# Kernel optimization log

Measured on AMD Instinct MI355X. Metric: run time of the kernel, lower is better.

The kernel has to match this reference:

```python
import jax, jax.numpy as jnp
import numpy as np

N_NODES = 100000
N_EDGES = 1600000
IN_DIM, HID_DIM, OUT_DIM = 64, 128, 1


def gcn_conv(x, W, b, src, dst, n_nodes):
    """PyG-style GCNConv: h = x @ W; out = D^-1/2 (A+I) D^-1/2 h + b.
    Self-loops handled analytically (message h_i * dinv_i^2) to avoid
    concatenating them onto the edge list."""
    h = x @ W  # [N, F_out]
    ones = jnp.ones((src.shape[0],), dtype=x.dtype)
    deg = jax.ops.segment_sum(ones, dst, num_segments=n_nodes) + 1.0  # +1 self-loop
    dinv = jax.lax.rsqrt(deg)  # deg >= 1 so always finite
    norm = dinv[src] * dinv[dst]  # [E]
    msgs = h[src] * norm[:, None]  # [E, F_out] gather + scale
    agg = jax.ops.segment_sum(msgs, dst, num_segments=n_nodes)  # scatter-add
    agg = agg + h * (dinv * dinv)[:, None]  # self-loop contribution
    return agg + b


def setup_inputs() -> dict:
    key = jax.random.key(0)
    k1, k2, k3, k4 = jax.random.split(key, 4)
    x = jax.random.normal(k1, (N_NODES, IN_DIM), dtype=jnp.float32)
    edge_index = jax.random.randint(k2, (2, N_EDGES), 0, N_NODES, dtype=jnp.int64)
    # Glorot-ish init for weights
    W1 = jax.random.normal(k3, (IN_DIM, HID_DIM), dtype=jnp.float32) / np.sqrt(IN_DIM)
    b1 = jnp.zeros((HID_DIM,), dtype=jnp.float32)
    W2 = jax.random.normal(k4, (HID_DIM, OUT_DIM), dtype=jnp.float32) / np.sqrt(HID_DIM)
    b2 = jnp.zeros((OUT_DIM,), dtype=jnp.float32)
    return {"x": x, "edge_index": edge_index, "W1": W1, "b1": b1, "W2": W2, "b2": b2}


def reference(x, edge_index, W1, b1, W2, b2):
    src, dst = edge_index[0], edge_index[1]
    h = gcn_conv(x, W1, b1, src, dst, N_NODES)
    h = jax.nn.relu(h)
    # dropout(0.3) in eval mode == identity
    out = gcn_conv(h, W2, b2, src, dst, N_NODES)
    return out.reshape(-1)  # [N]
```

## Files before the change

kernel.cpp:

```cpp
#include <hip/hip_runtime.h>
#include <hip/hip_bf16.h>

#define NNODES 100000
#define NEDGES 1600000
#define IN_DIM 64
#define HID_DIM 128

#define BUKSHIFT 7
#define BUKNODES 128
#define NBUK ((NNODES + 127) >> 7)
#define BUKCAP 2432
#define CHUNK 4096
#define TILE_N 128
#define W1TS 72
#define ACCS 66
#define QS 4096.0f

#define EPACK(s, d)  ((s) | (((d) & 127) << 24))
#define ESRC(p)      ((p) & 0x00FFFFFF)
#define EDL(p)       ((int)(((unsigned)(p)) >> 24))

typedef __attribute__((ext_vector_type(8))) short short8;
typedef __attribute__((ext_vector_type(4))) float f32x4;

__device__ inline unsigned short f2bf(float f) {
    unsigned u = __float_as_uint(f);
    u += 0x7fff + ((u >> 16) & 1);
    return (unsigned short)(u >> 16);
}
__device__ inline unsigned bfpack2(float a, float b) {
    return (unsigned)f2bf(a) | ((unsigned)f2bf(b) << 16);
}
__device__ inline int f2i12(float v) {
    float c = fminf(fmaxf(v * QS, -32767.f), 32767.f);
    return __float2int_rn(c);
}

__global__ __launch_bounds__(1024, 8) void k_part(const int* __restrict__ src,
                                                  const int* __restrict__ dst,
                                                  int* __restrict__ gbcur,
                                                  int* __restrict__ ebuf, int E) {
    __shared__ int stage[CHUNK];
    __shared__ unsigned short bukof[CHUNK];
    __shared__ int hist[NBUK];
    __shared__ int scanb[NBUK];
    __shared__ int basep[NBUK];
    __shared__ int sb[2][1024];
    int t = threadIdx.x;
    int start = blockIdx.x * CHUNK;
    int n = E - start; if (n > CHUNK) n = CHUNK;

    if (t < NBUK) hist[t] = 0;
    __syncthreads();

    int myb[4], myr[4], mp[4];
    #pragma unroll
    for (int i = 0; i < 4; i++) {
        int c = t + i * 1024;
        if (c < n) {
            int s = src[start + c];
            int d = dst[start + c];
            int b = d >> BUKSHIFT;
            myb[i] = b;
            mp[i]  = EPACK(s, d);
            myr[i] = atomicAdd(&hist[b], 1);
        } else myb[i] = -1;
    }
    __syncthreads();

    {
        int v = (t < NBUK) ? hist[t] : 0;
        sb[0][t] = v;
        __syncthreads();
        int pin = 0;
        for (int ofs = 1; ofs < 1024; ofs <<= 1) {
            sb[pin ^ 1][t] = (t >= ofs) ? sb[pin][t] + sb[pin][t - ofs] : sb[pin][t];
            __syncthreads();
            pin ^= 1;
        }
        if (t < NBUK) scanb[t] = sb[pin][t] - v;
    }

    if (t < NBUK) {
        int h = hist[t];
        basep[t] = h ? (t * BUKCAP + atomicAdd(&gbcur[t], h)) : 0;
    }
    __syncthreads();

    #pragma unroll
    for (int i = 0; i < 4; i++) {
        if (myb[i] >= 0) {
            int p = scanb[myb[i]] + myr[i];
            stage[p] = mp[i];
            bukof[p] = (unsigned short)myb[i];
        }
    }
    __syncthreads();

    for (int c = t; c < n; c += 1024) {
        int b = bukof[c];
        ebuf[basep[b] + (c - scanb[b])] = stage[c];
    }
}

__global__ __launch_bounds__(1024, 8) void k_bfill(const int* __restrict__ gbcur,
                                                   const int* __restrict__ ebuf,
                                                   const float* __restrict__ x,
                                                   int* __restrict__ off,
                                                   int* __restrict__ nend,
                                                   float* __restrict__ dinv,
                                                   int* __restrict__ csr,
                                                   short* __restrict__ xsq, int N) {
    __shared__ int sEdge[BUKCAP];
    __shared__ int lcnt[BUKNODES];
    __shared__ int sbuf[2][BUKNODES];
    __shared__ int cur[BUKNODES];
    __shared__ float sdinv[BUKNODES];
    int b = blockIdx.x, t = threadIdx.x;
    int nbase = b << BUKSHIFT;
    int rbase = b * BUKCAP;
    int cntb = gbcur[b];
    if (t < BUKNODES) lcnt[t] = 0;
    __syncthreads();
    for (int i = t; i < cntb; i += 1024) {
        int p = ebuf[rbase + i];
        sEdge[i] = p;
        atomicAdd(&lcnt[EDL(p)], 1);
    }
    __syncthreads();
    int v = (t < BUKNODES) ? lcnt[t] : 0;
    if (t < BUKNODES) sbuf[0][t] = v;
    __syncthreads();
    int pin = 0;
    for (int ofs = 1; ofs < BUKNODES; ofs <<= 1) {
        if (t < BUKNODES) sbuf[pin ^ 1][t] = (t >= ofs) ? sbuf[pin][t] + sbuf[pin][t - ofs]
                                                        : sbuf[pin][t];
        __syncthreads();
        pin ^= 1;
    }
    if (t < BUKNODES) {
        int o = rbase + sbuf[pin][t] - v;
        int nid = nbase + t;
        float dv = rsqrtf((float)v + 1.0f);
        sdinv[t] = dv;
        if (nid < N) {
            off[nid]  = o;
            nend[nid] = o + v;
            dinv[nid] = dv;
        }
        cur[t] = o;
    }
    __syncthreads();
    for (int i = t; i < cntb; i += 1024) {
        int p = sEdge[i];
        int pos = atomicAdd(&cur[EDL(p)], 1);
        csr[pos] = ESRC(p);
    }
    for (int i = t; i < BUKNODES * 16; i += 1024) {
        int nl = i >> 4;
        int nid = nbase + nl;
        if (nid < N) {
            float dv = sdinv[nl];
            float4 vx = ((const float4*)x)[(size_t)nid * 16 + (i & 15)];
            int q0 = f2i12(vx.x * dv), q1 = f2i12(vx.y * dv);
            int q2 = f2i12(vx.z * dv), q3 = f2i12(vx.w * dv);
            uint2 u;
            u.x = (q0 & 0xffff) | (q1 << 16);
            u.y = (q2 & 0xffff) | (q3 << 16);
            ((uint2*)xsq)[(size_t)nid * 16 + (i & 15)] = u;
        }
    }
}

__global__ __launch_bounds__(512, 8) void k_agg(const int* __restrict__ gbcur,
                                                const int* __restrict__ ebuf,
                                                const short* __restrict__ xsq,
                                                const float* __restrict__ dinv,
                                                unsigned short* __restrict__ aggu, int N) {
    __shared__ int acc[BUKNODES * ACCS];
    int b = blockIdx.x, t = threadIdx.x;
    int rbase = b * BUKCAP;
    int cntb = gbcur[b];
    for (int i = t; i < BUKNODES * ACCS; i += 512) acc[i] = 0;
    __syncthreads();

    int c = t & 7;
    int g = t >> 3;
    const uint4* xq4 = (const uint4*)xsq;
    for (int base = 0; base < cntb; base += 128) {
        int e0 = base + g, e1 = base + 64 + g;
        bool v0 = e0 < cntb, v1 = e1 < cntb;
        int p0 = v0 ? ebuf[rbase + e0] : 0;
        int p1 = v1 ? ebuf[rbase + e1] : 0;
        uint4 ua = {0, 0, 0, 0}, ub = {0, 0, 0, 0};
        if (v0) ua = xq4[(size_t)ESRC(p0) * 8 + c];
        if (v1) ub = xq4[(size_t)ESRC(p1) * 8 + c];
        if (v0) {
            int* ar = &acc[EDL(p0) * ACCS + c * 8];
            atomicAdd(&ar[0], (int)(short)(ua.x & 0xffff));
            atomicAdd(&ar[1], ((int)ua.x) >> 16);
            atomicAdd(&ar[2], (int)(short)(ua.y & 0xffff));
            atomicAdd(&ar[3], ((int)ua.y) >> 16);
            atomicAdd(&ar[4], (int)(short)(ua.z & 0xffff));
            atomicAdd(&ar[5], ((int)ua.z) >> 16);
            atomicAdd(&ar[6], (int)(short)(ua.w & 0xffff));
            atomicAdd(&ar[7], ((int)ua.w) >> 16);
        }
        if (v1) {
            int* ar = &acc[EDL(p1) * ACCS + c * 8];
            atomicAdd(&ar[0], (int)(short)(ub.x & 0xffff));
            atomicAdd(&ar[1], ((int)ub.x) >> 16);
            atomicAdd(&ar[2], (int)(short)(ub.y & 0xffff));
            atomicAdd(&ar[3], ((int)ub.y) >> 16);
            atomicAdd(&ar[4], (int)(short)(ub.z & 0xffff));
            atomicAdd(&ar[5], ((int)ub.z) >> 16);
            atomicAdd(&ar[6], (int)(short)(ub.w & 0xffff));
            atomicAdd(&ar[7], ((int)ub.w) >> 16);
        }
    }
    __syncthreads();

    int nbase = b << BUKSHIFT;
    for (int i = t; i < BUKNODES * 32; i += 512) {
        int dl = i >> 5, dp = i & 31;
        int n = nbase + dl;
        if (n < N) {
            float dd = dinv[n] * (1.0f / QS);
            int sp = ((const int*)xsq)[(size_t)n * 32 + dp];
            int s0 = (sp << 16) >> 16, s1 = sp >> 16;
            int A0 = acc[dl * ACCS + 2 * dp], A1 = acc[dl * ACCS + 2 * dp + 1];
            ((unsigned*)aggu)[(size_t)n * 32 + dp] =
                bfpack2((float)(A0 + s0) * dd, (float)(A1 + s1) * dd);
        }
    }
}

__global__ __launch_bounds__(512) void k_mlp(const uint4* __restrict__ aggb,
                                             const float* __restrict__ W1,
                                             const float* __restrict__ b1,
                                             const float* __restrict__ W2,
                                             const float* __restrict__ dinv,
                                             float* __restrict__ zd, int n_nodes) {
    __shared__ __align__(16) unsigned short sW1t[HID_DIM * W1TS];
    __shared__ float sW2[HID_DIM];
    __shared__ float sb1[HID_DIM];
    int t = threadIdx.x;
    for (int i = t; i < IN_DIM * HID_DIM; i += 512) {
        int k = i >> 7, hid = i & 127;
        sW1t[hid * W1TS + k] = f2bf(W1[i]);
    }
    if (t < HID_DIM) { sW2[t] = W2[t]; sb1[t] = b1[t]; }
    __syncthreads();

    int node0 = blockIdx.x * TILE_N;
    int w = t >> 6;
    int lane = t & 63;
    int col = lane & 15;
    int quad = lane >> 4;

    int na = node0 + w * 16 + col;
    int nac = na < n_nodes ? na : 0;
    const short8* arow = (const short8*)(aggb + (size_t)nac * 8);
    short8 a0 = arow[quad];
    short8 a1 = arow[4 + quad];

    float zpart[4] = {0, 0, 0, 0};
    #pragma unroll
    for (int h0 = 0; h0 < 8; h0++) {
        int hid = h0 * 16 + col;
        const short8* brow = (const short8*)(sW1t + hid * W1TS);
        short8 b0 = brow[quad];
        short8 b1f = brow[4 + quad];
        f32x4 cc = {0.f, 0.f, 0.f, 0.f};
        cc = __builtin_amdgcn_mfma_f32_16x16x32_bf16(a0, b0, cc, 0, 0, 0);
        cc = __builtin_amdgcn_mfma_f32_16x16x32_bf16(a1, b1f, cc, 0, 0, 0);
        float bb = sb1[hid], ww = sW2[hid];
        #pragma unroll
        for (int r = 0; r < 4; r++) {
            float v = cc[r] + bb;
            zpart[r] += (v > 0.f ? v : 0.f) * ww;
        }
    }
    #pragma unroll
    for (int m = 1; m < 16; m <<= 1) {
        #pragma unroll
        for (int r = 0; r < 4; r++) zpart[r] += __shfl_xor(zpart[r], m);
    }
    if (col == 0) {
        #pragma unroll
        for (int r = 0; r < 4; r++) {
            int n = node0 + w * 16 + quad * 4 + r;
            if (n < n_nodes) zd[n] = zpart[r] * dinv[n];
        }
    }
}

__global__ __launch_bounds__(1024, 8) void k_gather1(const int* __restrict__ off,
                                                     const int* __restrict__ nend,
                                                     const int* __restrict__ csr,
                                                     const float* __restrict__ zd,
                                                     const float* __restrict__ dinv,
                                                     const float* __restrict__ b2,
                                                     float* __restrict__ out, int n_nodes) {
    int tid = blockIdx.x * 1024 + threadIdx.x;
    int n = tid >> 3;
    int l = tid & 7;
    if (n >= n_nodes) return;
    int beg = off[n], fin = nend[n];
    float a0 = 0.0f, a1 = 0.0f;
    for (int i = beg + l; i < fin; i += 16) {
        a0 += zd[csr[i]];
        int i2 = i + 8;
        if (i2 < fin) a1 += zd[csr[i2]];
    }
    float a = a0 + a1;
    a += __shfl_xor(a, 1);
    a += __shfl_xor(a, 2);
    a += __shfl_xor(a, 4);
    if (l == 0) out[n] = (a + zd[n]) * dinv[n] + b2[0];
}

extern "C" void kernel_launch(void* const* d_in, const int* in_sizes, int n_in,
                              void* d_out, int out_size, void* d_ws, size_t ws_size,
                              hipStream_t stream) {
    const float* x  = (const float*)d_in[0];
    const int*   ei = (const int*)d_in[1];
    const float* W1 = (const float*)d_in[2];
    const float* b1 = (const float*)d_in[3];
    const float* W2 = (const float*)d_in[4];
    const float* b2 = (const float*)d_in[5];
    float* out = (float*)d_out;

    const int N = NNODES;
    const int E = NEDGES;
    const int* src = ei;
    const int* dst = ei + E;

    int* gbcur = (int*)d_ws;
    int* off   = gbcur + 1024;
    int* nend  = off + N;
    float* dinv = (float*)(nend + N);
    float* zd   = dinv + N;
    int* csr    = (int*)(zd + N);
    size_t o1 = ((size_t)((char*)(csr + NBUK * BUKCAP) - (char*)d_ws) + 127) & ~(size_t)127;
    short* xsq = (short*)((char*)d_ws + o1);
    size_t o2 = o1 + (size_t)N * 128;
    int* ebuf  = (int*)((char*)d_ws + o2);
    size_t o3 = ((o2 + (size_t)NBUK * BUKCAP * 4) + 127) & ~(size_t)127;
    unsigned short* aggu = (unsigned short*)((char*)d_ws + o3);

    hipMemsetAsync(gbcur, 0, 1024 * sizeof(int), stream);
    k_part<<<(E + CHUNK - 1) / CHUNK, 1024, 0, stream>>>(src, dst, gbcur, ebuf, E);
    k_bfill<<<NBUK, 1024, 0, stream>>>(gbcur, ebuf, x, off, nend, dinv, csr, xsq, N);
    k_agg<<<NBUK, 512, 0, stream>>>(gbcur, ebuf, xsq, dinv, aggu, N);
    k_mlp<<<(N + TILE_N - 1) / TILE_N, 512, 0, stream>>>((const uint4*)aggu, W1, b1, W2,
                                                         dinv, zd, N);
    k_gather1<<<(N * 8 + 1023) / 1024, 1024, 0, stream>>>(off, nend, csr, zd, dinv, b2, out, N);
}
```

Before: 175.8 us.

## Fuse bucket aggregation with MLP and prefetch next edge batch

Merges the layer-1 aggregation kernel with the MFMA MLP kernel. Each block's shared-memory accumulator is converted to bf16 in registers and fed straight into the MFMA, so the aggregated bf16 tensor is no longer written to and reread from global memory and one launch disappears. The edge loop is software-pipelined to load the next batch's indices and features before issuing the current batch's LDS atomics. The accumulator row stride changes to 65, and the larger shared footprint (W1 tile plus accumulator) lowers the occupancy hint to 6, which may reduce latency hiding.

```diff
diff --git a/kernel.cpp b/kernel.cpp
--- a/kernel.cpp
+++ b/kernel.cpp
@@ -11,9 +11,8 @@
 #define NBUK ((NNODES + 127) >> 7)
 #define BUKCAP 2432
 #define CHUNK 4096
-#define TILE_N 128
 #define W1TS 72
-#define ACCS 66
+#define ACCS 65
 #define QS 4096.0f
 
 #define EPACK(s, d)  ((s) | (((d) & 127) << 24))
@@ -34,6 +33,10 @@
 __device__ inline int f2i12(float v) {
     float c = fminf(fmaxf(v * QS, -32767.f), 32767.f);
     return __float2int_rn(c);
+}
+__device__ inline unsigned cvt2(int A0, int A1, int s01, float dd) {
+    int s0 = (s01 << 16) >> 16, s1 = s01 >> 16;
+    return bfpack2((float)(A0 + s0) * dd, (float)(A1 + s1) * dd);
 }
 
 __global__ __launch_bounds__(1024, 8) void k_part(const int* __restrict__ src,
@@ -172,97 +175,103 @@
     }
 }
 
-__global__ __launch_bounds__(512, 8) void k_agg(const int* __restrict__ gbcur,
-                                                const int* __restrict__ ebuf,
-                                                const short* __restrict__ xsq,
-                                                const float* __restrict__ dinv,
-                                                unsigned short* __restrict__ aggu, int N) {
+__global__ __launch_bounds__(512, 6) void k_aggmlp(const int* __restrict__ gbcur,
+                                                   const int* __restrict__ ebuf,
+                                                   const short* __restrict__ xsq,
+                                                   const float* __restrict__ dinv,
+                                                   const float* __restrict__ W1,
+                                                   const float* __restrict__ b1,
+                                                   const float* __restrict__ W2,
+                                                   float* __restrict__ zd, int N) {
     __shared__ int acc[BUKNODES * ACCS];
+    __shared__ __align__(16) unsigned short sW1t[HID_DIM * W1TS];
+    __shared__ float sW2[HID_DIM];
+    __shared__ float sb1[HID_DIM];
     int b = blockIdx.x, t = threadIdx.x;
     int rbase = b * BUKCAP;
     int cntb = gbcur[b];
+
     for (int i = t; i < BUKNODES * ACCS; i += 512) acc[i] = 0;
+    for (int i = t; i < IN_DIM * HID_DIM; i += 512) {
+        int k = i >> 7, hid = i & 127;
+        sW1t[hid * W1TS + k] = f2bf(W1[i]);
+    }
+    if (t < HID_DIM) { sW2[t] = W2[t]; sb1[t] = b1[t]; }
     __syncthreads();
 
     int c = t & 7;
     int g = t >> 3;
     const uint4* xq4 = (const uint4*)xsq;
+
+    int cp0 = 0, cp1 = 0; bool cv0 = false, cv1 = false;
+    uint4 cua = {0, 0, 0, 0}, cub = {0, 0, 0, 0};
+    if (cntb > 0) {
+        int e0 = g, e1 = 64 + g;
+        cv0 = e0 < cntb; cv1 = e1 < cntb;
+        cp0 = cv0 ? ebuf[rbase + e0] : 0;
+        cp1 = cv1 ? ebuf[rbase + e1] : 0;
+        if (cv0) cua = xq4[(size_t)ESRC(cp0) * 8 + c];
+        if (cv1) cub = xq4[(size_t)ESRC(cp1) * 8 + c];
+    }
     for (int base = 0; base < cntb; base += 128) {
-        int e0 = base + g, e1 = base + 64 + g;
-        bool v0 = e0 < cntb, v1 = e1 < cntb;
-        int p0 = v0 ? ebuf[rbase + e0] : 0;
-        int p1 = v1 ? ebuf[rbase + e1] : 0;
-        uint4 ua = {0, 0, 0, 0}, ub = {0, 0, 0, 0};
-        if (v0) ua = xq4[(size_t)ESRC(p0) * 8 + c];
-        if (v1) ub = xq4[(size_t)ESRC(p1) * 8 + c];
-        if (v0) {
-            int* ar = &acc[EDL(p0) * ACCS + c * 8];
-            atomicAdd(&ar[0], (int)(short)(ua.x & 0xffff));
-            atomicAdd(&ar[1], ((int)ua.x) >> 16);
-            atomicAdd(&ar[2], (int)(short)(ua.y & 0xffff));
-            atomicAdd(&ar[3], ((int)ua.y) >> 16);
-            atomicAdd(&ar[4], (int)(short)(ua.z & 0xffff));
-            atomicAdd(&ar[5], ((int)ua.z) >> 16);
-            atomicAdd(&ar[6], (int)(short)(ua.w & 0xffff));
-            atomicAdd(&ar[7], ((int)ua.w) >> 16);
-        }
-        if (v1) {
-            int* ar = &acc[EDL(p1) * ACCS + c * 8];
-            atomicAdd(&ar[0], (int)(short)(ub.x & 0xffff));
-            atomicAdd(&ar[1], ((int)ub.x) >> 16);
-            atomicAdd(&ar[2], (int)(short)(ub.y & 0xffff));
-            atomicAdd(&ar[3], ((int)ub.y) >> 16);
-            atomicAdd(&ar[4], (int)(short)(ub.z & 0xffff));
-            atomicAdd(&ar[5], ((int)ub.z) >> 16);
-            atomicAdd(&ar[6], (int)(short)(ub.w & 0xffff));
-            atomicAdd(&ar[7], ((int)ub.w) >> 16);
-        }
-    }
-    __syncthreads();
-
-    int nbase = b << BUKSHIFT;
-    for (int i = t; i < BUKNODES * 32; i += 512) {
-        int dl = i >> 5, dp = i & 31;
-        int n = nbase + dl;
-        if (n < N) {
-            float dd = dinv[n] * (1.0f / QS);
-            int sp = ((const int*)xsq)[(size_t)n * 32 + dp];
-            int s0 = (sp << 16) >> 16, s1 = sp >> 16;
-            int A0 = acc[dl * ACCS + 2 * dp], A1 = acc[dl * ACCS + 2 * dp + 1];
-            ((unsigned*)aggu)[(size_t)n * 32 + dp] =
-                bfpack2((float)(A0 + s0) * dd, (float)(A1 + s1) * dd);
-        }
-    }
-}
-
-__global__ __launch_bounds__(512) void k_mlp(const uint4* __restrict__ aggb,
-                                             const float* __restrict__ W1,
-                                             const float* __restrict__ b1,
-                                             const float* __restrict__ W2,
-                                             const float* __restrict__ dinv,
-                                             float* __restrict__ zd, int n_nodes) {
-    __shared__ __align__(16) unsigned short sW1t[HID_DIM * W1TS];
-    __shared__ float sW2[HID_DIM];
-    __shared__ float sb1[HID_DIM];
-    int t = threadIdx.x;
-    for (int i = t; i < IN_DIM * HID_DIM; i += 512) {
-        int k = i >> 7, hid = i & 127;
-        sW1t[hid * W1TS + k] = f2bf(W1[i]);
-    }
-    if (t < HID_DIM) { sW2[t] = W2[t]; sb1[t] = b1[t]; }
-    __syncthreads();
-
-    int node0 = blockIdx.x * TILE_N;
-    int w = t >> 6;
-    int lane = t & 63;
-    int col = lane & 15;
-    int quad = lane >> 4;
-
+        int nb = base + 128;
+        int np0 = 0, np1 = 0; bool nv0 = false, nv1 = false;
+        uint4 nua = {0, 0, 0, 0}, nub = {0, 0, 0, 0};
+        if (nb < cntb) {
+            int e0 = nb + g, e1 = nb + 64 + g;
+            nv0 = e0 < cntb; nv1 = e1 < cntb;
+            np0 = nv0 ? ebuf[rbase + e0] : 0;
+            np1 = nv1 ? ebuf[rbase + e1] : 0;
+            if (nv0) nua = xq4[(size_t)ESRC(np0) * 8 + c];
+            if (nv1) nub = xq4[(size_t)ESRC(np1) * 8 + c];
+        }
+        if (cv0) {
+            int* ar = &acc[EDL(cp0) * ACCS + c * 8];
+            atomicAdd(&ar[0], (int)(short)(cua.x & 0xffff));
+            atomicAdd(&ar[1], ((int)cua.x) >> 16);
+            atomicAdd(&ar[2], (int)(short)(cua.y & 0xffff));
+            atomicAdd(&ar[3], ((int)cua.y) >> 16);
+            atomicAdd(&ar[4], (int)(short)(cua.z & 0xffff));
+            atomicAdd(&ar[5], ((int)cua.z) >> 16);
+            atomicAdd(&ar[6], (int)(short)(cua.w & 0xffff));
+            atomicAdd(&ar[7], ((int)cua.w) >> 16);
+        }
+        if (cv1) {
+            int* ar = &acc[EDL(cp1) * ACCS + c * 8];
+            atomicAdd(&ar[0], (int)(short)(cub.x & 0xffff));
+            atomicAdd(&ar[1], ((int)cub.x) >> 16);
+            atomicAdd(&ar[2], (int)(short)(cub.y & 0xffff));
+            atomicAdd(&ar[3], ((int)cub.y) >> 16);
+            atomicAdd(&ar[4], (int)(short)(cub.z & 0xffff));
+            atomicAdd(&ar[5], ((int)cub.z) >> 16);
+            atomicAdd(&ar[6], (int)(short)(cub.w & 0xffff));
+            atomicAdd(&ar[7], ((int)cub.w) >> 16);
+        }
+        cp0 = np0; cp1 = np1; cv0 = nv0; cv1 = nv1; cua = nua; cub = nub;
+    }
+    __syncthreads();
+
+    int w = t >> 6, lane = t & 63;
+    int col = lane & 15, quad = lane >> 4;
+    int node0 = b << BUKSHIFT;
     int na = node0 + w * 16 + col;
-    int nac = na < n_nodes ? na : 0;
-    const short8* arow = (const short8*)(aggb + (size_t)nac * 8);
-    short8 a0 = arow[quad];
-    short8 a1 = arow[4 + quad];
+    int nac = na < N ? na : N - 1;
+    float dd = dinv[nac] * (1.0f / QS);
+
+    int nl = w * 16 + col;
+    const int* arow = &acc[nl * ACCS];
+    uint4 s0 = xq4[(size_t)nac * 8 + quad];
+    uint4 s1 = xq4[(size_t)nac * 8 + 4 + quad];
+    int j0 = quad * 8;
+    union { unsigned u[4]; short8 v; } A0, A1;
+    A0.u[0] = cvt2(arow[j0 + 0], arow[j0 + 1], (int)s0.x, dd);
+    A0.u[1] = cvt2(arow[j0 + 2], arow[j0 + 3], (int)s0.y, dd);
+    A0.u[2] = cvt2(arow[j0 + 4], arow[j0 + 5], (int)s0.z, dd);
+    A0.u[3] = cvt2(arow[j0 + 6], arow[j0 + 7], (int)s0.w, dd);
+    A1.u[0] = cvt2(arow[32 + j0 + 0], arow[32 + j0 + 1], (int)s1.x, dd);
+    A1.u[1] = cvt2(arow[32 + j0 + 2], arow[32 + j0 + 3], (int)s1.y, dd);
+    A1.u[2] = cvt2(arow[32 + j0 + 4], arow[32 + j0 + 5], (int)s1.z, dd);
+    A1.u[3] = cvt2(arow[32 + j0 + 6], arow[32 + j0 + 7], (int)s1.w, dd);
 
     float zpart[4] = {0, 0, 0, 0};
     #pragma unroll
@@ -272,8 +281,8 @@
         short8 b0 = brow[quad];
         short8 b1f = brow[4 + quad];
         f32x4 cc = {0.f, 0.f, 0.f, 0.f};
-        cc = __builtin_amdgcn_mfma_f32_16x16x32_bf16(a0, b0, cc, 0, 0, 0);
-        cc = __builtin_amdgcn_mfma_f32_16x16x32_bf16(a1, b1f, cc, 0, 0, 0);
+        cc = __builtin_amdgcn_mfma_f32_16x16x32_bf16(A0.v, b0, cc, 0, 0, 0);
+        cc = __builtin_amdgcn_mfma_f32_16x16x32_bf16(A1.v, b1f, cc, 0, 0, 0);
         float bb = sb1[hid], ww = sW2[hid];
         #pragma unroll
         for (int r = 0; r < 4; r++) {
@@ -290,7 +299,7 @@
         #pragma unroll
         for (int r = 0; r < 4; r++) {
             int n = node0 + w * 16 + quad * 4 + r;
-            if (n < n_nodes) zd[n] = zpart[r] * dinv[n];
+            if (n < N) zd[n] = zpart[r] * dinv[n];
         }
     }
 }
@@ -346,14 +355,10 @@
     short* xsq = (short*)((char*)d_ws + o1);
     size_t o2 = o1 + (size_t)N * 128;
     int* ebuf  = (int*)((char*)d_ws + o2);
-    size_t o3 = ((o2 + (size_t)NBUK * BUKCAP * 4) + 127) & ~(size_t)127;
-    unsigned short* aggu = (unsigned short*)((char*)d_ws + o3);
 
     hipMemsetAsync(gbcur, 0, 1024 * sizeof(int), stream);
     k_part<<<(E + CHUNK - 1) / CHUNK, 1024, 0, stream>>>(src, dst, gbcur, ebuf, E);
     k_bfill<<<NBUK, 1024, 0, stream>>>(gbcur, ebuf, x, off, nend, dinv, csr, xsq, N);
-    k_agg<<<NBUK, 512, 0, stream>>>(gbcur, ebuf, xsq, dinv, aggu, N);
-    k_mlp<<<(N + TILE_N - 1) / TILE_N, 512, 0, stream>>>((const uint4*)aggu, W1, b1, W2,
-                                                         dinv, zd, N);
+    k_aggmlp<<<NBUK, 512, 0, stream>>>(gbcur, ebuf, xsq, dinv, W1, b1, W2, zd, N);
     k_gather1<<<(N * 8 + 1023) / 1024, 1024, 0, stream>>>(off, nend, csr, zd, dinv, b2, out, N);
 }
```

Result: faster. 172.2 us (-2.0%).
